# Performance work log

Measured on AMD Instinct MI355X. Metric: run time of the kernel, lower is better.

Reference implementation:

```python
import jax, jax.numpy as jnp
import numpy as np

N_HEAD = 16
D_MODEL = 1024


def setup_inputs() -> dict:
    key = jax.random.key(0)
    k1, k2, k3, k4, k5, k6 = jax.random.split(key, 6)
    B, S, D = 2, 2048, D_MODEL
    src = jax.random.normal(k1, (B, S, D), dtype=jnp.float32)
    attn_mask = jax.random.uniform(k2, (B, S, S), dtype=jnp.float32)
    # torch nn.Linear(d, 3d) / nn.Linear(d, d) params; stored as (in, out) for x @ W
    scale = 1.0 / np.sqrt(D)
    W_qkv = jax.random.uniform(k3, (D, 3 * D), dtype=jnp.float32, minval=-scale, maxval=scale)
    b_qkv = jax.random.uniform(k4, (3 * D,), dtype=jnp.float32, minval=-scale, maxval=scale)
    W_out = jax.random.uniform(k5, (D, D), dtype=jnp.float32, minval=-scale, maxval=scale)
    b_out = jax.random.uniform(k6, (D,), dtype=jnp.float32, minval=-scale, maxval=scale)
    return {"src": src, "attn_mask": attn_mask, "W_qkv": W_qkv, "b_qkv": b_qkv,
            "W_out": W_out, "b_out": b_out}


def reference(src, attn_mask, W_qkv, b_qkv, W_out, b_out):
    B, S, D = src.shape
    H = N_HEAD
    dh = D // H
    # broadcast mask [B,S,S] -> [B,1,S,S] (matches torch unsqueeze(1))
    mask = attn_mask[:, None, :, :]
    qkv = src @ W_qkv + b_qkv                      # [B,S,3D]
    q, k, v = jnp.split(qkv, 3, axis=-1)
    q = q.reshape(B, S, H, dh).transpose(0, 2, 1, 3)   # [B,H,S,dh]
    k = k.reshape(B, S, H, dh).transpose(0, 2, 1, 3)
    v = v.reshape(B, S, H, dh).transpose(0, 2, 1, 3)
    scores = jnp.einsum('bhqd,bhkd->bhqk', q, k) * (float(dh) ** -0.5)
    scores = scores * mask + (mask - 1.0) * 10000.0
    weights = jax.nn.softmax(scores, axis=-1)      # dropout_p=0 -> identity in eval/train
    out = jnp.einsum('bhqk,bhkd->bhqd', weights, v)
    out = out.transpose(0, 2, 1, 3).reshape(B, S, D)
    return out @ W_out + b_out
```

## Files before the change

### kernel.cpp

```cpp
#include <hip/hip_runtime.h>
#include <stdint.h>

#define SEQ    2048
#define DMODEL 1024

typedef __bf16 bf16x8 __attribute__((ext_vector_type(8)));
typedef float  f32x4  __attribute__((ext_vector_type(4)));

typedef __attribute__((address_space(1))) const void CGV;
typedef __attribute__((address_space(3))) void LDSV;

__device__ __forceinline__ void load_lds16(const void* g, void* l) {
    __builtin_amdgcn_global_load_lds((CGV*)g, (LDSV*)l, 16, 0, 0);
}

__global__ __launch_bounds__(256)
void transpose_f32_to_bf16(const float* __restrict__ in, __bf16* __restrict__ out,
                           int R, int C)
{
    __shared__ float tile[32][33];
    const int t  = threadIdx.x;
    const int tx = t & 31, ty = t >> 5;
    const int c0 = blockIdx.x * 32;
    const int r0 = blockIdx.y * 32;
#pragma unroll
    for (int i = 0; i < 4; ++i)
        tile[ty + i * 8][tx] = in[(size_t)(r0 + ty + i * 8) * C + c0 + tx];
    __syncthreads();
#pragma unroll
    for (int i = 0; i < 4; ++i)
        out[(size_t)(c0 + ty + i * 8) * R + r0 + tx] = (__bf16)tile[tx][ty + i * 8];
}

__global__ __launch_bounds__(256)
void convert_f32_to_bf16(const float* __restrict__ in, __bf16* __restrict__ out)
{
    const int i = (blockIdx.x * 256 + threadIdx.x) * 8;
    float4 a = *(const float4*)(in + i);
    float4 b = *(const float4*)(in + i + 4);
    __bf16 tmp[8] = { (__bf16)a.x, (__bf16)a.y, (__bf16)a.z, (__bf16)a.w,
                      (__bf16)b.x, (__bf16)b.y, (__bf16)b.z, (__bf16)b.w };
    *(uint4*)(out + i) = *(uint4*)tmp;
}

__global__ __launch_bounds__(256)
void transpose_v(const __bf16* __restrict__ in, __bf16* __restrict__ out)
{
    __shared__ __bf16 tile[32][34];
    const int t  = threadIdx.x;
    const int tx = t & 31, ty = t >> 5;
    const int s0 = blockIdx.x * 32;
    const int d0 = blockIdx.y * 32;
    const int bh = blockIdx.z;
    const __bf16* ip = in  + (size_t)bh * SEQ * 64;
    __bf16*       op = out + (size_t)bh * 64 * SEQ;
#pragma unroll
    for (int i = 0; i < 4; ++i)
        tile[ty + i * 8][tx] = ip[(size_t)(s0 + ty + i * 8) * 64 + d0 + tx];
    __syncthreads();
#pragma unroll
    for (int i = 0; i < 4; ++i)
        op[(size_t)(d0 + ty + i * 8) * SEQ + s0 + tx] = tile[tx][ty + i * 8];
}

template<bool A_IS_F32>
__global__ __launch_bounds__(256)
void gemm_kernel(const void* __restrict__ Av, const __bf16* __restrict__ Bt,
                 const float* __restrict__ bias,
                 __bf16* __restrict__ Cq, __bf16* __restrict__ Ck,
                 __bf16* __restrict__ Cv, float* __restrict__ Cplain,
                 int K, int N, int mode)
{
    __shared__ __attribute__((aligned(16))) __bf16 As[128][32];
    __shared__ __attribute__((aligned(16))) __bf16 Bs[128][32];

    const int t    = threadIdx.x;
    const int wave = __builtin_amdgcn_readfirstlane(t >> 6);
    const int lane = t & 63;
    const int l15  = lane & 15;
    const int quad = lane >> 4;
    const int wm   = (wave >> 1) * 64;
    const int wn   = (wave & 1) * 64;
    const int m0   = blockIdx.y * 128;
    const int n0   = blockIdx.x * 128;

    const int arow  = lane >> 2;
    const int akoff = (lane & 3) * 8;

    f32x4 acc[4][4] = {};

    for (int k0 = 0; k0 < K; k0 += 32) {
        __syncthreads();
        if (A_IS_F32) {
            const float* A = (const float*)Av;
            int row = t >> 1, kk = (t & 1) * 16;
            const float* srcp = A + (size_t)(m0 + row) * K + k0 + kk;
            float4 v0 = *(const float4*)(srcp);
            float4 v1 = *(const float4*)(srcp + 4);
            float4 v2 = *(const float4*)(srcp + 8);
            float4 v3 = *(const float4*)(srcp + 12);
            __bf16 tmp[16] = {
                (__bf16)v0.x, (__bf16)v0.y, (__bf16)v0.z, (__bf16)v0.w,
                (__bf16)v1.x, (__bf16)v1.y, (__bf16)v1.z, (__bf16)v1.w,
                (__bf16)v2.x, (__bf16)v2.y, (__bf16)v2.z, (__bf16)v2.w,
                (__bf16)v3.x, (__bf16)v3.y, (__bf16)v3.z, (__bf16)v3.w };
            *(uint4*)(&As[row][kk])     = *(uint4*)(tmp);
            *(uint4*)(&As[row][kk + 8]) = *(uint4*)(tmp + 8);
        } else {
            const __bf16* A = (const __bf16*)Av;
#pragma unroll
            for (int p = 0; p < 2; ++p) {
                int slab = (wave * 2 + p) * 16;
                const __bf16* g = A + (size_t)(m0 + slab + arow) * K + k0 + akoff;
                load_lds16(g, &As[slab][0]);
            }
        }
#pragma unroll
        for (int p = 0; p < 2; ++p) {
            int slab = (wave * 2 + p) * 16;
            const __bf16* g = Bt + (size_t)(n0 + slab + arow) * K + k0 + akoff;
            load_lds16(g, &Bs[slab][0]);
        }
        __syncthreads();

        bf16x8 af[4], bfr[4];
#pragma unroll
        for (int mi = 0; mi < 4; ++mi)
            af[mi] = *(const bf16x8*)(&As[wm + mi * 16 + l15][quad * 8]);
#pragma unroll
        for (int ni = 0; ni < 4; ++ni)
            bfr[ni] = *(const bf16x8*)(&Bs[wn + ni * 16 + l15][quad * 8]);
#pragma unroll
        for (int mi = 0; mi < 4; ++mi)
#pragma unroll
            for (int ni = 0; ni < 4; ++ni)
                acc[mi][ni] = __builtin_amdgcn_mfma_f32_16x16x32_bf16(
                    af[mi], bfr[ni], acc[mi][ni], 0, 0, 0);
    }

#pragma unroll
    for (int mi = 0; mi < 4; ++mi) {
        int rowb = m0 + wm + mi * 16 + quad * 4;
#pragma unroll
        for (int ni = 0; ni < 4; ++ni) {
            int col = n0 + wn + ni * 16 + l15;
            float bia = bias[col];
#pragma unroll
            for (int r = 0; r < 4; ++r) {
                float v = acc[mi][ni][r] + bia;
                int rr = rowb + r;
                if (mode == 0) {
                    int b = rr >> 11;
                    int s = rr & 2047;
                    int part = col >> 10;
                    int rem  = col & 1023;
                    int h = rem >> 6;
                    int d = rem & 63;
                    __bf16* dst = (part == 0) ? Cq : (part == 1) ? Ck : Cv;
                    dst[(((size_t)(b * 16 + h)) * SEQ + s) * 64 + d] = (__bf16)v;
                } else {
                    Cplain[(size_t)rr * N + col] = v;
                }
            }
        }
    }
}

__global__ __launch_bounds__(256, 4)
void attn_kernel(const __bf16* __restrict__ Q, const __bf16* __restrict__ Kb,
                 const __bf16* __restrict__ Vtg, const float* __restrict__ mask,
                 __bf16* __restrict__ Out)
{
    __shared__ __attribute__((aligned(16))) __bf16 Kt[2][64 * 64];
    __shared__ __attribute__((aligned(16))) __bf16 Vt[2][64 * 64];
    __shared__ __attribute__((aligned(16))) __bf16 Ps[4][16 * 64];

    const int t    = threadIdx.x;
    const int wave = __builtin_amdgcn_readfirstlane(t >> 6);
    const int lane = t & 63;
    const int l15  = lane & 15;
    const int quad = lane >> 4;
    const int swq  = lane & 7;
    const int bh   = blockIdx.x;
    const int b    = bh >> 4;
    const int h    = bh & 15;
    const int q0   = blockIdx.y * 64 + wave * 16;

    const __bf16* Qp  = Q   + (size_t)bh * SEQ * 64;
    const __bf16* Kp  = Kb  + (size_t)bh * SEQ * 64;
    const __bf16* Vtp = Vtg + (size_t)bh * 64 * SEQ;
    const float*  Mrow = mask + (size_t)b * SEQ * SEQ + (size_t)(q0 + l15) * SEQ + quad * 4;

    const int ch  = wave * 2;
    const int rw0 = ch * 8 + (lane >> 3);
    const int swz = ((lane & 7) ^ (lane >> 3)) * 8;
    const __bf16* kS0 = Kp  + (size_t)rw0 * 64 + swz;
    const __bf16* kS1 = Kp  + (size_t)(rw0 + 8) * 64 + swz;
    const __bf16* vS0 = Vtp + (size_t)rw0 * SEQ + swz;
    const __bf16* vS1 = Vtp + (size_t)(rw0 + 8) * SEQ + swz;

    bf16x8 qf[2];
#pragma unroll
    for (int ks = 0; ks < 2; ++ks)
        qf[ks] = *(const bf16x8*)(Qp + (size_t)(q0 + l15) * 64 + ks * 32 + quad * 8);

    f32x4 oacc[4] = {};
    float mrun = -1e30f, lrun = 0.f;

    load_lds16(kS0, &Kt[0][ch * 512]);
    load_lds16(kS1, &Kt[0][(ch + 1) * 512]);
    load_lds16(vS0, &Vt[0][ch * 512]);
    load_lds16(vS1, &Vt[0][(ch + 1) * 512]);
    f32x4 mk[4];
#pragma unroll
    for (int nb = 0; nb < 4; ++nb)
        mk[nb] = *(const f32x4*)(Mrow + nb * 16);

    const char* PsW = (const char*)&Ps[wave][0] + l15 * 128;

#pragma unroll 2
    for (int tt = 0; tt < SEQ / 64; ++tt) {
        const int key0 = tt * 64;
        const int keyn = (key0 + 64 <= SEQ - 64) ? key0 + 64 : SEQ - 64;
        const int cur  = tt & 1;
        const char* kcur = (const char*)&Kt[cur][0];
        const char* vcur = (const char*)&Vt[cur][0];
        __bf16* knxt = &Kt[cur ^ 1][0];
        __bf16* vnxt = &Vt[cur ^ 1][0];

        asm volatile("s_waitcnt vmcnt(0)" ::: "memory");
        __builtin_amdgcn_s_barrier();
        __builtin_amdgcn_sched_barrier(0);

        load_lds16(kS0 + (size_t)keyn * 64, knxt + ch * 512);
        load_lds16(kS1 + (size_t)keyn * 64, knxt + (ch + 1) * 512);
        load_lds16(vS0 + keyn, vnxt + ch * 512);
        load_lds16(vS1 + keyn, vnxt + (ch + 1) * 512);
        __builtin_amdgcn_sched_barrier(0);

        f32x4 sa[4];
#pragma unroll
        for (int nb = 0; nb < 4; ++nb) {
            const char* kb = kcur + (nb * 16 + l15) * 128;
            bf16x8 kf0 = *(const bf16x8*)(kb + (((quad) ^ swq) << 4));
            bf16x8 kf1 = *(const bf16x8*)(kb + (((4 + quad) ^ swq) << 4));
            f32x4 z = {};
            z = __builtin_amdgcn_mfma_f32_16x16x32_bf16(kf0, qf[0], z, 0, 0, 0);
            z = __builtin_amdgcn_mfma_f32_16x16x32_bf16(kf1, qf[1], z, 0, 0, 0);
            sa[nb] = z;
        }

#pragma unroll
        for (int nb = 0; nb < 4; ++nb)
#pragma unroll
            for (int r = 0; r < 4; ++r) {
                float m  = mk[nb][r];
                float tt2 = __fmaf_rn(0.125f, sa[nb][r], 10000.0f);
                sa[nb][r] = __fmaf_rn(m, tt2, -10000.0f);
            }
#pragma unroll
        for (int nb = 0; nb < 4; ++nb)
            mk[nb] = *(const f32x4*)(Mrow + keyn + nb * 16);

        float vmax = -1e30f;
#pragma unroll
        for (int nb = 0; nb < 4; ++nb)
#pragma unroll
            for (int r = 0; r < 4; ++r)
                vmax = fmaxf(vmax, sa[nb][r]);
        vmax = fmaxf(vmax, __shfl_xor(vmax, 16));
        vmax = fmaxf(vmax, __shfl_xor(vmax, 32));
        float mnew  = fmaxf(mrun, vmax);
        float alpha = __expf(mrun - mnew);
        mrun = mnew;

        float accs = 0.f;
#pragma unroll
        for (int nb = 0; nb < 4; ++nb)
#pragma unroll
            for (int r = 0; r < 4; ++r) {
                float p = __expf(sa[nb][r] - mnew);
                sa[nb][r] = p;
                accs += p;
            }
        accs += __shfl_xor(accs, 16);
        accs += __shfl_xor(accs, 32);
        lrun = lrun * alpha + accs;

#pragma unroll
        for (int nb = 0; nb < 4; ++nb) {
            union { __bf16 hh[4]; uint2 u; } pk;
            pk.hh[0] = (__bf16)sa[nb][0];
            pk.hh[1] = (__bf16)sa[nb][1];
            pk.hh[2] = (__bf16)sa[nb][2];
            pk.hh[3] = (__bf16)sa[nb][3];
            *(uint2*)(PsW + (((nb * 2 + (quad >> 1)) ^ swq) << 4) + (quad & 1) * 8) = pk.u;
        }
        asm volatile("s_waitcnt lgkmcnt(0)" ::: "memory");
        __builtin_amdgcn_sched_barrier(0);

        float a4[4];
#pragma unroll
        for (int r = 0; r < 4; ++r)
            a4[r] = __shfl(alpha, quad * 4 + r);
#pragma unroll
        for (int cb = 0; cb < 4; ++cb)
#pragma unroll
            for (int r = 0; r < 4; ++r)
                oacc[cb][r] *= a4[r];

        bf16x8 pf0 = *(const bf16x8*)(PsW + (((quad) ^ swq) << 4));
        bf16x8 pf1 = *(const bf16x8*)(PsW + (((4 + quad) ^ swq) << 4));

        __builtin_amdgcn_s_setprio(1);
#pragma unroll
        for (int cb = 0; cb < 4; ++cb) {
            const char* vb = vcur + (cb * 16 + l15) * 128;
            bf16x8 vf0 = *(const bf16x8*)(vb + (((quad) ^ swq) << 4));
            bf16x8 vf1 = *(const bf16x8*)(vb + (((4 + quad) ^ swq) << 4));
            oacc[cb] = __builtin_amdgcn_mfma_f32_16x16x32_bf16(pf0, vf0, oacc[cb], 0, 0, 0);
            oacc[cb] = __builtin_amdgcn_mfma_f32_16x16x32_bf16(pf1, vf1, oacc[cb], 0, 0, 0);
        }
        __builtin_amdgcn_s_setprio(0);
    }

    float l4[4];
#pragma unroll
    for (int r = 0; r < 4; ++r)
        l4[r] = __shfl(lrun, quad * 4 + r);
#pragma unroll
    for (int cb = 0; cb < 4; ++cb) {
#pragma unroll
        for (int r = 0; r < 4; ++r) {
            int qq = q0 + quad * 4 + r;
            float v = oacc[cb][r] / l4[r];
            Out[((size_t)(b * SEQ + qq)) * DMODEL + h * 64 + cb * 16 + l15] = (__bf16)v;
        }
    }
}

extern "C" void kernel_launch(void* const* d_in, const int* in_sizes, int n_in,
                              void* d_out, int out_size, void* d_ws, size_t ws_size,
                              hipStream_t stream)
{
    const float* src  = nullptr;
    const float* mask = nullptr;
    const float* Wqkv = nullptr;
    const float* bqkv = nullptr;
    const float* Wout = nullptr;
    const float* bout = nullptr;
    for (int i = 0; i < n_in; ++i) {
        switch (in_sizes[i]) {
            case 4194304: src  = (const float*)d_in[i]; break;
            case 8388608: mask = (const float*)d_in[i]; break;
            case 3145728: Wqkv = (const float*)d_in[i]; break;
            case 3072:    bqkv = (const float*)d_in[i]; break;
            case 1048576: Wout = (const float*)d_in[i]; break;
            case 1024:    bout = (const float*)d_in[i]; break;
        }
    }
    float* out = (float*)d_out;

    const size_t NE = (size_t)2 * 16 * SEQ * 64;
    __bf16* Qb     = (__bf16*)d_ws;
    __bf16* Kb     = Qb + NE;
    __bf16* Vb     = Kb + NE;
    __bf16* Vtg    = Vb + NE;
    __bf16* Wqkv_t = Vtg + NE;
    __bf16* Wout_t = Wqkv_t + (size_t)3072 * 1024;
    __bf16* Ao     = Vb;
    __bf16* SrcBf  = Vtg;

    transpose_f32_to_bf16<<<dim3(3072 / 32, 1024 / 32), 256, 0, stream>>>(
        Wqkv, Wqkv_t, 1024, 3072);
    transpose_f32_to_bf16<<<dim3(1024 / 32, 1024 / 32), 256, 0, stream>>>(
        Wout, Wout_t, 1024, 1024);

    convert_f32_to_bf16<<<dim3(4194304 / (256 * 8)), 256, 0, stream>>>(src, SrcBf);

    gemm_kernel<false><<<dim3(3072 / 128, 4096 / 128), 256, 0, stream>>>(
        (const void*)SrcBf, Wqkv_t, bqkv, Qb, Kb, Vb, nullptr, 1024, 3072, 0);

    transpose_v<<<dim3(SEQ / 32, 2, 32), 256, 0, stream>>>(Vb, Vtg);

    attn_kernel<<<dim3(32, SEQ / 64), 256, 0, stream>>>(Qb, Kb, Vtg, mask, Ao);

    gemm_kernel<false><<<dim3(1024 / 128, 4096 / 128), 256, 0, stream>>>(
        (const void*)Ao, Wout_t, bout, nullptr, nullptr, nullptr, out, 1024, 1024, 1);
}
```

Measured before the change: 262.9 us.

## Process two query tiles per wave with exp2 softmax and lazy rescaling

Each wave now handles 32 query rows instead of 16, so every K/V tile loaded into LDS is reused across twice as many rows and the grid is halved. The softmax folds log2(e) into the scale and mask constants so it can use exp2 directly. It also skips rescaling the output accumulator unless the running max grows by more than a threshold. This trades more registers per thread (launch bounds relaxed to 2) and fewer blocks for less global/LDS traffic per query row and fewer exponentials.

```diff
diff --git a/kernel.cpp b/kernel.cpp
--- a/kernel.cpp
+++ b/kernel.cpp
@@ -13,6 +13,8 @@
 __device__ __forceinline__ void load_lds16(const void* g, void* l) {
     __builtin_amdgcn_global_load_lds((CGV*)g, (LDSV*)l, 16, 0, 0);
 }
+
+__device__ __forceinline__ float fast_exp2(float x) { return __builtin_exp2f(x); }
 
 __global__ __launch_bounds__(256)
 void transpose_f32_to_bf16(const float* __restrict__ in, __bf16* __restrict__ out,
@@ -166,14 +168,14 @@
     }
 }
 
-__global__ __launch_bounds__(256, 4)
+__global__ __launch_bounds__(256, 2)
 void attn_kernel(const __bf16* __restrict__ Q, const __bf16* __restrict__ Kb,
                  const __bf16* __restrict__ Vtg, const float* __restrict__ mask,
                  __bf16* __restrict__ Out)
 {
     __shared__ __attribute__((aligned(16))) __bf16 Kt[2][64 * 64];
     __shared__ __attribute__((aligned(16))) __bf16 Vt[2][64 * 64];
-    __shared__ __attribute__((aligned(16))) __bf16 Ps[4][16 * 64];
+    __shared__ __attribute__((aligned(16))) __bf16 Ps[4][32 * 64];
 
     const int t    = threadIdx.x;
     const int wave = __builtin_amdgcn_readfirstlane(t >> 6);
@@ -184,12 +186,16 @@
     const int bh   = blockIdx.x;
     const int b    = bh >> 4;
     const int h    = bh & 15;
-    const int q0   = blockIdx.y * 64 + wave * 16;
+    const int q0   = blockIdx.y * 128 + wave * 32;
+
+    const float C1 = 0.180336880f;
+    const float C2 = 14426.9502f;
 
     const __bf16* Qp  = Q   + (size_t)bh * SEQ * 64;
     const __bf16* Kp  = Kb  + (size_t)bh * SEQ * 64;
     const __bf16* Vtp = Vtg + (size_t)bh * 64 * SEQ;
-    const float*  Mrow = mask + (size_t)b * SEQ * SEQ + (size_t)(q0 + l15) * SEQ + quad * 4;
+    const float*  Mrow0 = mask + (size_t)b * SEQ * SEQ + (size_t)(q0 + l15) * SEQ + quad * 4;
+    const float*  Mrow1 = Mrow0 + (size_t)16 * SEQ;
 
     const int ch  = wave * 2;
     const int rw0 = ch * 8 + (lane >> 3);
@@ -199,24 +205,29 @@
     const __bf16* vS0 = Vtp + (size_t)rw0 * SEQ + swz;
     const __bf16* vS1 = Vtp + (size_t)(rw0 + 8) * SEQ + swz;
 
-    bf16x8 qf[2];
-#pragma unroll
-    for (int ks = 0; ks < 2; ++ks)
-        qf[ks] = *(const bf16x8*)(Qp + (size_t)(q0 + l15) * 64 + ks * 32 + quad * 8);
-
-    f32x4 oacc[4] = {};
-    float mrun = -1e30f, lrun = 0.f;
+    bf16x8 qf00, qf01, qf10, qf11;
+    qf00 = *(const bf16x8*)(Qp + (size_t)(q0 + l15) * 64 + quad * 8);
+    qf01 = *(const bf16x8*)(Qp + (size_t)(q0 + l15) * 64 + 32 + quad * 8);
+    qf10 = *(const bf16x8*)(Qp + (size_t)(q0 + 16 + l15) * 64 + quad * 8);
+    qf11 = *(const bf16x8*)(Qp + (size_t)(q0 + 16 + l15) * 64 + 32 + quad * 8);
+
+    f32x4 oacc0[4] = {}, oacc1[4] = {};
+    float mrun0 = -1e30f, lrun0 = 0.f;
+    float mrun1 = -1e30f, lrun1 = 0.f;
 
     load_lds16(kS0, &Kt[0][ch * 512]);
     load_lds16(kS1, &Kt[0][(ch + 1) * 512]);
     load_lds16(vS0, &Vt[0][ch * 512]);
     load_lds16(vS1, &Vt[0][(ch + 1) * 512]);
-    f32x4 mk[4];
-#pragma unroll
-    for (int nb = 0; nb < 4; ++nb)
-        mk[nb] = *(const f32x4*)(Mrow + nb * 16);
-
-    const char* PsW = (const char*)&Ps[wave][0] + l15 * 128;
+    f32x4 mk0[4], mk1[4];
+#pragma unroll
+    for (int nb = 0; nb < 4; ++nb) {
+        mk0[nb] = *(const f32x4*)(Mrow0 + nb * 16);
+        mk1[nb] = *(const f32x4*)(Mrow1 + nb * 16);
+    }
+
+    const char* PsW0 = (const char*)&Ps[wave][0] + l15 * 128;
+    const char* PsW1 = PsW0 + 16 * 128;
 
 #pragma unroll 2
     for (int tt = 0; tt < SEQ / 64; ++tt) {
@@ -238,79 +249,113 @@
         load_lds16(vS1 + keyn, vnxt + (ch + 1) * 512);
         __builtin_amdgcn_sched_barrier(0);
 
-        f32x4 sa[4];
+        f32x4 sa0[4], sa1[4];
 #pragma unroll
         for (int nb = 0; nb < 4; ++nb) {
             const char* kb = kcur + (nb * 16 + l15) * 128;
             bf16x8 kf0 = *(const bf16x8*)(kb + (((quad) ^ swq) << 4));
             bf16x8 kf1 = *(const bf16x8*)(kb + (((4 + quad) ^ swq) << 4));
-            f32x4 z = {};
-            z = __builtin_amdgcn_mfma_f32_16x16x32_bf16(kf0, qf[0], z, 0, 0, 0);
-            z = __builtin_amdgcn_mfma_f32_16x16x32_bf16(kf1, qf[1], z, 0, 0, 0);
-            sa[nb] = z;
+            f32x4 z0 = {}, z1 = {};
+            z0 = __builtin_amdgcn_mfma_f32_16x16x32_bf16(kf0, qf00, z0, 0, 0, 0);
+            z1 = __builtin_amdgcn_mfma_f32_16x16x32_bf16(kf0, qf10, z1, 0, 0, 0);
+            z0 = __builtin_amdgcn_mfma_f32_16x16x32_bf16(kf1, qf01, z0, 0, 0, 0);
+            z1 = __builtin_amdgcn_mfma_f32_16x16x32_bf16(kf1, qf11, z1, 0, 0, 0);
+            sa0[nb] = z0;
+            sa1[nb] = z1;
         }
 
 #pragma unroll
         for (int nb = 0; nb < 4; ++nb)
 #pragma unroll
             for (int r = 0; r < 4; ++r) {
-                float m  = mk[nb][r];
-                float tt2 = __fmaf_rn(0.125f, sa[nb][r], 10000.0f);
-                sa[nb][r] = __fmaf_rn(m, tt2, -10000.0f);
+                float t0 = __fmaf_rn(C1, sa0[nb][r], C2);
+                float t1 = __fmaf_rn(C1, sa1[nb][r], C2);
+                sa0[nb][r] = __fmaf_rn(mk0[nb][r], t0, -C2);
+                sa1[nb][r] = __fmaf_rn(mk1[nb][r], t1, -C2);
             }
 #pragma unroll
+        for (int nb = 0; nb < 4; ++nb) {
+            mk0[nb] = *(const f32x4*)(Mrow0 + keyn + nb * 16);
+            mk1[nb] = *(const f32x4*)(Mrow1 + keyn + nb * 16);
+        }
+
+        float v0 = fmaxf(fmaxf(sa0[0][0], sa0[0][1]), fmaxf(sa0[0][2], sa0[0][3]));
+        float v1 = fmaxf(fmaxf(sa1[0][0], sa1[0][1]), fmaxf(sa1[0][2], sa1[0][3]));
+#pragma unroll
+        for (int nb = 1; nb < 4; ++nb) {
+            v0 = fmaxf(v0, fmaxf(fmaxf(sa0[nb][0], sa0[nb][1]), fmaxf(sa0[nb][2], sa0[nb][3])));
+            v1 = fmaxf(v1, fmaxf(fmaxf(sa1[nb][0], sa1[nb][1]), fmaxf(sa1[nb][2], sa1[nb][3])));
+        }
+        v0 = fmaxf(v0, __shfl_xor(v0, 16));
+        v1 = fmaxf(v1, __shfl_xor(v1, 16));
+        v0 = fmaxf(v0, __shfl_xor(v0, 32));
+        v1 = fmaxf(v1, __shfl_xor(v1, 32));
+
+        float al0 = 1.f, al1 = 1.f;
+        bool need = (v0 > mrun0 + 8.f) || (v1 > mrun1 + 8.f);
+        if (__any(need)) {
+            float nm0 = fmaxf(mrun0, v0);
+            float nm1 = fmaxf(mrun1, v1);
+            al0 = fast_exp2(mrun0 - nm0);
+            al1 = fast_exp2(mrun1 - nm1);
+            mrun0 = nm0;
+            mrun1 = nm1;
+            float a0[4], a1[4];
+#pragma unroll
+            for (int r = 0; r < 4; ++r) {
+                a0[r] = __shfl(al0, quad * 4 + r);
+                a1[r] = __shfl(al1, quad * 4 + r);
+            }
+#pragma unroll
+            for (int cb = 0; cb < 4; ++cb)
+#pragma unroll
+                for (int r = 0; r < 4; ++r) {
+                    oacc0[cb][r] *= a0[r];
+                    oacc1[cb][r] *= a1[r];
+                }
+        }
+
+        float ac0 = 0.f, ac1 = 0.f;
+#pragma unroll
         for (int nb = 0; nb < 4; ++nb)
-            mk[nb] = *(const f32x4*)(Mrow + keyn + nb * 16);
-
-        float vmax = -1e30f;
-#pragma unroll
-        for (int nb = 0; nb < 4; ++nb)
-#pragma unroll
-            for (int r = 0; r < 4; ++r)
-                vmax = fmaxf(vmax, sa[nb][r]);
-        vmax = fmaxf(vmax, __shfl_xor(vmax, 16));
-        vmax = fmaxf(vmax, __shfl_xor(vmax, 32));
-        float mnew  = fmaxf(mrun, vmax);
-        float alpha = __expf(mrun - mnew);
-        mrun = mnew;
-
-        float accs = 0.f;
-#pragma unroll
-        for (int nb = 0; nb < 4; ++nb)
 #pragma unroll
             for (int r = 0; r < 4; ++r) {
-                float p = __expf(sa[nb][r] - mnew);
-                sa[nb][r] = p;
-                accs += p;
+                float p0 = fast_exp2(sa0[nb][r] - mrun0);
+                float p1 = fast_exp2(sa1[nb][r] - mrun1);
+                sa0[nb][r] = p0;
+                sa1[nb][r] = p1;
+                ac0 += p0;
+                ac1 += p1;
             }
-        accs += __shfl_xor(accs, 16);
-        accs += __shfl_xor(accs, 32);
-        lrun = lrun * alpha + accs;
+        ac0 += __shfl_xor(ac0, 16);
+        ac1 += __shfl_xor(ac1, 16);
+        ac0 += __shfl_xor(ac0, 32);
+        ac1 += __shfl_xor(ac1, 32);
+        lrun0 = lrun0 * al0 + ac0;
+        lrun1 = lrun1 * al1 + ac1;
 
 #pragma unroll
         for (int nb = 0; nb < 4; ++nb) {
-            union { __bf16 hh[4]; uint2 u; } pk;
-            pk.hh[0] = (__bf16)sa[nb][0];
-            pk.hh[1] = (__bf16)sa[nb][1];
-            pk.hh[2] = (__bf16)sa[nb][2];
-            pk.hh[3] = (__bf16)sa[nb][3];
-            *(uint2*)(PsW + (((nb * 2 + (quad >> 1)) ^ swq) << 4) + (quad & 1) * 8) = pk.u;
+            union { __bf16 hh[4]; uint2 u; } p0, p1;
+            p0.hh[0] = (__bf16)sa0[nb][0];
+            p0.hh[1] = (__bf16)sa0[nb][1];
+            p0.hh[2] = (__bf16)sa0[nb][2];
+            p0.hh[3] = (__bf16)sa0[nb][3];
+            p1.hh[0] = (__bf16)sa1[nb][0];
+            p1.hh[1] = (__bf16)sa1[nb][1];
+            p1.hh[2] = (__bf16)sa1[nb][2];
+            p1.hh[3] = (__bf16)sa1[nb][3];
+            const int so = (((nb * 2 + (quad >> 1)) ^ swq) << 4) + (quad & 1) * 8;
+            *(uint2*)(PsW0 + so) = p0.u;
+            *(uint2*)(PsW1 + so) = p1.u;
         }
         asm volatile("s_waitcnt lgkmcnt(0)" ::: "memory");
         __builtin_amdgcn_sched_barrier(0);
 
-        float a4[4];
-#pragma unroll
-        for (int r = 0; r < 4; ++r)
-            a4[r] = __shfl(alpha, quad * 4 + r);
-#pragma unroll
-        for (int cb = 0; cb < 4; ++cb)
-#pragma unroll
-            for (int r = 0; r < 4; ++r)
-                oacc[cb][r] *= a4[r];
-
-        bf16x8 pf0 = *(const bf16x8*)(PsW + (((quad) ^ swq) << 4));
-        bf16x8 pf1 = *(const bf16x8*)(PsW + (((4 + quad) ^ swq) << 4));
+        bf16x8 pf00 = *(const bf16x8*)(PsW0 + (((quad) ^ swq) << 4));
+        bf16x8 pf01 = *(const bf16x8*)(PsW0 + (((4 + quad) ^ swq) << 4));
+        bf16x8 pf10 = *(const bf16x8*)(PsW1 + (((quad) ^ swq) << 4));
+        bf16x8 pf11 = *(const bf16x8*)(PsW1 + (((4 + quad) ^ swq) << 4));
 
         __builtin_amdgcn_s_setprio(1);
 #pragma unroll
@@ -318,23 +363,29 @@
             const char* vb = vcur + (cb * 16 + l15) * 128;
             bf16x8 vf0 = *(const bf16x8*)(vb + (((quad) ^ swq) << 4));
             bf16x8 vf1 = *(const bf16x8*)(vb + (((4 + quad) ^ swq) << 4));
-            oacc[cb] = __builtin_amdgcn_mfma_f32_16x16x32_bf16(pf0, vf0, oacc[cb], 0, 0, 0);
-            oacc[cb] = __builtin_amdgcn_mfma_f32_16x16x32_bf16(pf1, vf1, oacc[cb], 0, 0, 0);
+            oacc0[cb] = __builtin_amdgcn_mfma_f32_16x16x32_bf16(pf00, vf0, oacc0[cb], 0, 0, 0);
+            oacc1[cb] = __builtin_amdgcn_mfma_f32_16x16x32_bf16(pf10, vf0, oacc1[cb], 0, 0, 0);
+            oacc0[cb] = __builtin_amdgcn_mfma_f32_16x16x32_bf16(pf01, vf1, oacc0[cb], 0, 0, 0);
+            oacc1[cb] = __builtin_amdgcn_mfma_f32_16x16x32_bf16(pf11, vf1, oacc1[cb], 0, 0, 0);
         }
         __builtin_amdgcn_s_setprio(0);
     }
 
-    float l4[4];
-#pragma unroll
-    for (int r = 0; r < 4; ++r)
-        l4[r] = __shfl(lrun, quad * 4 + r);
+    float l40[4], l41[4];
+#pragma unroll
+    for (int r = 0; r < 4; ++r) {
+        l40[r] = __shfl(lrun0, quad * 4 + r);
+        l41[r] = __shfl(lrun1, quad * 4 + r);
+    }
 #pragma unroll
     for (int cb = 0; cb < 4; ++cb) {
 #pragma unroll
         for (int r = 0; r < 4; ++r) {
-            int qq = q0 + quad * 4 + r;
-            float v = oacc[cb][r] / l4[r];
-            Out[((size_t)(b * SEQ + qq)) * DMODEL + h * 64 + cb * 16 + l15] = (__bf16)v;
+            int qq0 = q0 + quad * 4 + r;
+            Out[((size_t)(b * SEQ + qq0)) * DMODEL + h * 64 + cb * 16 + l15] =
+                (__bf16)(oacc0[cb][r] / l40[r]);
+            Out[((size_t)(b * SEQ + qq0 + 16)) * DMODEL + h * 64 + cb * 16 + l15] =
+                (__bf16)(oacc1[cb][r] / l41[r]);
         }
     }
 }
@@ -383,7 +434,7 @@
 
     transpose_v<<<dim3(SEQ / 32, 2, 32), 256, 0, stream>>>(Vb, Vtg);
 
-    attn_kernel<<<dim3(32, SEQ / 64), 256, 0, stream>>>(Qb, Kb, Vtg, mask, Ao);
+    attn_kernel<<<dim3(32, SEQ / 128), 256, 0, stream>>>(Qb, Kb, Vtg, mask, Ao);
 
     gemm_kernel<false><<<dim3(1024 / 128, 4096 / 128), 256, 0, stream>>>(
         (const void*)Ao, Wout_t, bout, nullptr, nullptr, nullptr, out, 1024, 1024, 1);
```

Result: slower. 270.4 us (+2.9%).
